# Optimization experiments

Measured on AMD Instinct MI355X. Metric: run time of the kernel, lower is better.

## Reference

```python
import jax, jax.numpy as jnp
import numpy as np

B, S, H, M, E = 64, 512, 1024, 26, 676  # batch, seq, hidden, max_nodes, max_edges (M*M)


def setup_inputs() -> dict:
    key = jax.random.key(0)
    ks = jax.random.split(key, 16)
    seq = jax.random.normal(ks[0], (B, S, H), jnp.float32)
    # ragged, strictly-increasing sentence-end offsets in [1, S-1], zero-padded tail
    rng = np.random.RandomState(0)
    off = np.zeros((B, M - 1), np.int64)
    for b in range(B):
        c = rng.randint(5, M)  # count of valid offsets per sample (ragged)
        off[b, :c] = np.sort(rng.choice(np.arange(1, S), size=c, replace=False))
    s = 1.0 / np.sqrt(H)
    s3 = 1.0 / np.sqrt(3 * H)
    return {
        'sequence_outputs': seq,
        'proof_offsets': jnp.asarray(off),
        'node_labels': jax.random.randint(ks[1], (B, M), 0, 2),
        'edge_labels': jax.random.randint(ks[2], (B, E), 0, 2),
        'W_naf': jax.random.normal(ks[3], (H, H), jnp.float32) * s,
        'b_naf': jnp.zeros((H,), jnp.float32),
        'W_cd': jax.random.normal(ks[4], (H, H), jnp.float32) * s,
        'b_cd': jnp.zeros((H,), jnp.float32),
        'W_co': jax.random.normal(ks[5], (H, 2), jnp.float32) * s,
        'b_co': jnp.zeros((2,), jnp.float32),
        'W_nd': jax.random.normal(ks[6], (H, H), jnp.float32) * s,
        'b_nd': jnp.zeros((H,), jnp.float32),
        'W_no': jax.random.normal(ks[7], (H, 2), jnp.float32) * s,
        'b_no': jnp.zeros((2,), jnp.float32),
        'W_ed': jax.random.normal(ks[8], (3 * H, H), jnp.float32) * s3,
        'b_ed': jnp.zeros((H,), jnp.float32),
        'W_eo': jax.random.normal(ks[9], (H, 2), jnp.float32) * s,
        'b_eo': jnp.zeros((2,), jnp.float32),
    }


def reference(sequence_outputs, proof_offsets, node_labels, edge_labels,
              W_naf, b_naf, W_cd, b_cd, W_co, b_co,
              W_nd, b_nd, W_no, b_no, W_ed, b_ed, W_eo, b_eo):
    Bx, Sx, Hx = sequence_outputs.shape
    Mx = node_labels.shape[1]
    Ex = edge_labels.shape[1]

    cls = sequence_outputs[:, 0, :]                       # [B,H]
    naf = cls @ W_naf + b_naf                             # NAF node embedding
    logits = jnp.tanh(cls @ W_cd + b_cd) @ W_co + b_co    # RobertaClassificationHead (eval: dropout=id)

    # segment-mean pooling via inclusive prefix sums: segment j = tokens (prev_j, off_j]
    P = jnp.cumsum(sequence_outputs, axis=1)              # [B,S,H]
    off = proof_offsets                                   # [B,M-1]
    prev = jnp.concatenate([jnp.zeros((Bx, 1), off.dtype), off[:, :-1]], axis=1)
    valid = off > 0                                       # [B,M-1]
    seg_sum = (jnp.take_along_axis(P, off[..., None], axis=1)
               - jnp.take_along_axis(P, prev[..., None], axis=1))  # [B,M-1,H]
    seg_len = jnp.maximum(off - prev, 1).astype(sequence_outputs.dtype)
    seg_mean = seg_sum / seg_len[..., None] * valid[..., None]

    count = valid.sum(axis=1)                             # nodes per sample (excl. NAF)
    # node embeddings: seg means at 0..count-1, NAF at index count, zeros after
    node_full = jnp.concatenate([seg_mean, jnp.zeros((Bx, 1, Hx), seg_mean.dtype)], axis=1)  # [B,M,H]
    idx = jnp.arange(Mx)
    node_full = node_full + (idx[None, :, None] == count[:, None, None]) * naf[:, None, :]

    # all-pairs edge features over n=count+1 nodes, row-major flat k=i*n+j, zero-padded to E
    n = count + 1                                         # [B]
    k = jnp.arange(Ex)                                    # [E]
    i = jnp.clip(k[None, :] // n[:, None], 0, Mx - 1)     # [B,E]
    j = jnp.clip(k[None, :] % n[:, None], 0, Mx - 1)
    valid_e = (k[None, :] < (n * n)[:, None])[..., None]
    ni = jnp.take_along_axis(node_full, i[..., None], axis=1)  # [B,E,H]
    nj = jnp.take_along_axis(node_full, j[..., None], axis=1)
    edge = jnp.concatenate([nj, ni, nj - ni], axis=-1) * valid_e  # [B,E,3H]

    node_logits = jnp.tanh(node_full @ W_nd + b_nd) @ W_no + b_no
    edge_logits = jnp.tanh(edge @ W_ed + b_ed) @ W_eo + b_eo
    return (logits, node_logits, edge_logits)
```

## Files before the change

### kernel.cpp

```cpp
#include <hip/hip_runtime.h>
#include <hip/hip_bf16.h>

#define B_ 64
#define S_ 512
#define H_ 1024
#define M_ 26
#define E_ 676

typedef short bf16x8 __attribute__((ext_vector_type(8)));
typedef float f32x4 __attribute__((ext_vector_type(4)));

__device__ __forceinline__ void gload16(const void* g, void* l) {
    __builtin_amdgcn_global_load_lds((const __attribute__((address_space(1))) unsigned int*)g,
                                     (__attribute__((address_space(3))) unsigned int*)l,
                                     16, 0, 0);
}

__device__ __forceinline__ float tanh_fast(float x) {
    float e = __expf(2.0f * x);
    return 1.0f - 2.0f * __builtin_amdgcn_rcpf(e + 1.0f);
}

__global__ void k_prep(const float* __restrict__ Wnd, const float* __restrict__ Wed,
                       __hip_bfloat16* __restrict__ Wt) {
    __shared__ float T[32][33];
    int bx = blockIdx.x, by = blockIdx.y, s = blockIdx.z;
    int t = threadIdx.x;
    int c = t & 31, r0 = t >> 5;
    const int HH = H_ * H_;
#pragma unroll
    for (int i = 0; i < 4; ++i) {
        int r = r0 + 8 * i;
        size_t k = by * 32 + r, n = bx * 32 + c;
        float v;
        if (s == 0)      v = Wnd[k * H_ + n];
        else if (s == 1) v = Wed[k * H_ + n] + Wed[2 * HH + k * H_ + n];
        else             v = Wed[HH + k * H_ + n] - Wed[2 * HH + k * H_ + n];
        T[r][c] = v;
    }
    __syncthreads();
#pragma unroll
    for (int i = 0; i < 4; ++i) {
        int rr = r0 + 8 * i;
        Wt[(size_t)(s * H_ + bx * 32 + rr) * H_ + by * 32 + c] = __float2bfloat16(T[c][rr]);
    }
}

__global__ void k_init(const float* __restrict__ bnaf, const float* __restrict__ bcd,
                       float* __restrict__ naf, float* __restrict__ cdh,
                       const int* __restrict__ off, int* __restrict__ count,
                       const float* __restrict__ bed, const float* __restrict__ Weo,
                       const float* __restrict__ beo, float* __restrict__ econ) {
    __shared__ float s0[256], s1[256];
    int bx = blockIdx.x;
    if (bx < 256) {
        int i = bx * 256 + threadIdx.x;
        naf[i] = bnaf[i & (H_ - 1)];
    } else if (bx < 512) {
        int i = (bx - 256) * 256 + threadIdx.x;
        cdh[i] = bcd[i & (H_ - 1)];
    } else if (bx == 512) {
        if (threadIdx.x < 64) {
            int b = threadIdx.x;
            int c = 0;
            for (int m = 0; m < M_ - 1; ++m) c += (off[b * (M_ - 1) + m] > 0) ? 1 : 0;
            count[b] = c;
        }
    } else {
        int tid = threadIdx.x;
        float a0 = 0.f, a1 = 0.f;
        for (int h = tid; h < H_; h += 256) {
            float t = tanh_fast(bed[h]);
            a0 += t * Weo[h * 2 + 0];
            a1 += t * Weo[h * 2 + 1];
        }
        s0[tid] = a0; s1[tid] = a1; __syncthreads();
        for (int o = 128; o > 0; o >>= 1) {
            if (tid < o) { s0[tid] += s0[tid + o]; s1[tid] += s1[tid + o]; }
            __syncthreads();
        }
        if (tid == 0) { econ[0] = s0[0] + beo[0]; econ[1] = s1[0] + beo[1]; }
    }
}

__global__ __launch_bounds__(256) void k_cls2(const float* __restrict__ seq,
                                              const float* __restrict__ Wnaf,
                                              const float* __restrict__ Wcd,
                                              float* __restrict__ naf,
                                              float* __restrict__ cdh) {
    __shared__ float As[16][64];
    __shared__ float Bs[16][64];
    int tid = threadIdx.x;
    int bx = blockIdx.x;
    int kbase = blockIdx.y * 128;
    const float* W;
    float* dst;
    int cbase;
    if (bx < 16) { W = Wnaf; dst = naf; cbase = bx * 64; }
    else         { W = Wcd;  dst = cdh; cbase = (bx - 16) * 64; }
    int tx = tid % 16, ty = tid / 16;
    float c[4][4] = {};
    int la_row = tid / 4;
    int la_k4  = (tid % 4) * 4;
    int lb_k   = tid / 16;
    int lb_c4  = (tid % 16) * 4;
    for (int k0 = 0; k0 < 128; k0 += 16) {
        float4 a = *(const float4*)(seq + (size_t)la_row * S_ * H_ + kbase + k0 + la_k4);
        *(float4*)(&Bs[lb_k][lb_c4]) =
            *(const float4*)(W + (size_t)(kbase + k0 + lb_k) * H_ + cbase + lb_c4);
        As[la_k4 + 0][la_row] = a.x;
        As[la_k4 + 1][la_row] = a.y;
        As[la_k4 + 2][la_row] = a.z;
        As[la_k4 + 3][la_row] = a.w;
        __syncthreads();
#pragma unroll
        for (int kk = 0; kk < 16; ++kk) {
            float4 av = *(const float4*)(&As[kk][ty * 4]);
            float4 bv = *(const float4*)(&Bs[kk][tx * 4]);
            c[0][0] += av.x * bv.x; c[0][1] += av.x * bv.y; c[0][2] += av.x * bv.z; c[0][3] += av.x * bv.w;
            c[1][0] += av.y * bv.x; c[1][1] += av.y * bv.y; c[1][2] += av.y * bv.z; c[1][3] += av.y * bv.w;
            c[2][0] += av.z * bv.x; c[2][1] += av.z * bv.y; c[2][2] += av.z * bv.z; c[2][3] += av.z * bv.w;
            c[3][0] += av.w * bv.x; c[3][1] += av.w * bv.y; c[3][2] += av.w * bv.z; c[3][3] += av.w * bv.w;
        }
        __syncthreads();
    }
#pragma unroll
    for (int i = 0; i < 4; ++i)
#pragma unroll
        for (int j = 0; j < 4; ++j)
            atomicAdd(dst + (size_t)(ty * 4 + i) * H_ + cbase + tx * 4 + j, c[i][j]);
}

__global__ void k_logits(const float* __restrict__ cdh, const float* __restrict__ Wco,
                         const float* __restrict__ bco, float* __restrict__ out) {
    int b = blockIdx.x, tid = threadIdx.x;
    float a0 = 0.f, a1 = 0.f;
    for (int h = tid; h < H_; h += 256) {
        float t = tanh_fast(cdh[(size_t)b * H_ + h]);
        a0 += t * Wco[h * 2 + 0];
        a1 += t * Wco[h * 2 + 1];
    }
    __shared__ float s0[256], s1[256];
    s0[tid] = a0; s1[tid] = a1; __syncthreads();
    for (int o = 128; o > 0; o >>= 1) {
        if (tid < o) { s0[tid] += s0[tid + o]; s1[tid] += s1[tid + o]; }
        __syncthreads();
    }
    if (tid == 0) { out[b * 2 + 0] = s0[0] + bco[0]; out[b * 2 + 1] = s1[0] + bco[1]; }
}

__global__ void k_seg(const float* __restrict__ seq, const int* __restrict__ off,
                      float* __restrict__ node_sum) {
    int b = blockIdx.y;
    int chunk = blockIdx.x;
    __shared__ int offs[M_ - 1];
    __shared__ int c_s, offmax_s;
    int tid = threadIdx.x;
    if (tid < M_ - 1) offs[tid] = off[b * (M_ - 1) + tid];
    __syncthreads();
    if (tid == 0) {
        int c = 0;
        while (c < M_ - 1 && offs[c] > 0) c++;
        c_s = c; offmax_s = (c > 0) ? offs[c - 1] : 0;
    }
    __syncthreads();
    int c = c_s, offmax = offmax_s;
    int t0 = chunk * 32;
    int ts = max(t0, 1), te = min(t0 + 31, offmax);
    if (ts > te) return;
    int m = 0;
    while (m < c && offs[m] < ts) m++;
    const float4* sq = (const float4*)(seq + (size_t)b * S_ * H_);
    float4 acc = make_float4(0, 0, 0, 0);
    for (int t = ts; t <= te; ++t) {
        if (offs[m] < t) {
            float* dst = node_sum + ((size_t)(b * M_ + m)) * H_ + tid * 4;
            atomicAdd(dst + 0, acc.x); atomicAdd(dst + 1, acc.y);
            atomicAdd(dst + 2, acc.z); atomicAdd(dst + 3, acc.w);
            acc = make_float4(0, 0, 0, 0);
            while (offs[m] < t) m++;
        }
        float4 v = sq[(size_t)t * (H_ / 4) + tid];
        acc.x += v.x; acc.y += v.y; acc.z += v.z; acc.w += v.w;
    }
    float* dst = node_sum + ((size_t)(b * M_ + m)) * H_ + tid * 4;
    atomicAdd(dst + 0, acc.x); atomicAdd(dst + 1, acc.y);
    atomicAdd(dst + 2, acc.z); atomicAdd(dst + 3, acc.w);
}

__global__ void k_finalize(const float* __restrict__ sums, const int* __restrict__ off,
                           const int* __restrict__ count, const float* __restrict__ naf,
                           __hip_bfloat16* __restrict__ nodeB) {
    int b = blockIdx.y, m = blockIdx.x, tid = threadIdx.x;
    int cnt = count[b];
    float4 v = make_float4(0, 0, 0, 0);
    const float4* row = (const float4*)(sums + ((size_t)(b * M_ + m)) * H_);
    if (m < M_ - 1) {
        int o = off[b * (M_ - 1) + m];
        if (o > 0) {
            int prev = (m > 0) ? off[b * (M_ - 1) + m - 1] : 0;
            float inv = 1.0f / (float)max(o - prev, 1);
            float4 s = row[tid];
            v = make_float4(s.x * inv, s.y * inv, s.z * inv, s.w * inv);
        }
    }
    if (m == cnt) {
        float4 a = ((const float4*)(naf + (size_t)b * H_))[tid];
        v.x += a.x; v.y += a.y; v.z += a.z; v.w += a.w;
    }
    __hip_bfloat16 __attribute__((aligned(8))) h[4] = {
        __float2bfloat16(v.x), __float2bfloat16(v.y),
        __float2bfloat16(v.z), __float2bfloat16(v.w)};
    *(ushort4*)(nodeB + ((size_t)(b * M_ + m)) * H_ + tid * 4) = *(const ushort4*)h;
}

#define GM 1664
#define GN 3072
#define GK 1024
__global__ __launch_bounds__(256) void k_mfma(const __hip_bfloat16* __restrict__ A,
                                              const __hip_bfloat16* __restrict__ Bt,
                                              float* __restrict__ C) {
    __shared__ __hip_bfloat16 As[128 * 32];
    __shared__ __hip_bfloat16 Bs[128 * 32];
    int tid = threadIdx.x;
    int wid = tid >> 6, ln = tid & 63;
    int row0 = blockIdx.y * 128, col0 = blockIdx.x * 128;
    const __hip_bfloat16* ga = A + (size_t)(row0 + wid * 16 + (ln >> 2)) * GK + (ln & 3) * 8;
    const __hip_bfloat16* gb = Bt + (size_t)(col0 + wid * 16 + (ln >> 2)) * GK + (ln & 3) * 8;
    __hip_bfloat16* lA = As + wid * 512;
    __hip_bfloat16* lB = Bs + wid * 512;
    int mrow = (wid >> 1) * 64, ncol = (wid & 1) * 64;
    int l15 = ln & 15, l4 = ln >> 4;
    f32x4 acc[4][4] = {};
    const __hip_bfloat16* pa = As + (size_t)(mrow + l15) * 32 + l4 * 8;
    const __hip_bfloat16* pb = Bs + (size_t)(ncol + l15) * 32 + l4 * 8;
    for (int k0 = 0; k0 < GK; k0 += 32) {
        gload16(ga, lA);
        gload16(ga + 64 * GK, lA + 2048);
        gload16(gb, lB);
        gload16(gb + 64 * GK, lB + 2048);
        ga += 32; gb += 32;
        __syncthreads();
        bf16x8 af[4], bf[4];
#pragma unroll
        for (int mi = 0; mi < 4; ++mi) af[mi] = *(const bf16x8*)(pa + mi * 16 * 32);
#pragma unroll
        for (int ni = 0; ni < 4; ++ni) bf[ni] = *(const bf16x8*)(pb + ni * 16 * 32);
#pragma unroll
        for (int mi = 0; mi < 4; ++mi)
#pragma unroll
            for (int ni = 0; ni < 4; ++ni)
                acc[mi][ni] = __builtin_amdgcn_mfma_f32_16x16x32_bf16(af[mi], bf[ni],
                                                                      acc[mi][ni], 0, 0, 0);
        __syncthreads();
    }
#pragma unroll
    for (int mi = 0; mi < 4; ++mi)
#pragma unroll
        for (int ni = 0; ni < 4; ++ni) {
            f32x4 v = acc[mi][ni];
            size_t r = row0 + mrow + mi * 16 + l4 * 4;
            size_t cc = col0 + ncol + ni * 16 + l15;
            C[(r + 0) * GN + cc] = v[0];
            C[(r + 1) * GN + cc] = v[1];
            C[(r + 2) * GN + cc] = v[2];
            C[(r + 3) * GN + cc] = v[3];
        }
}

__global__ void k_node_logits(const float* __restrict__ Cm, const float* __restrict__ bnd,
                              const float* __restrict__ Wno, const float* __restrict__ bno,
                              float* __restrict__ out) {
    int r = blockIdx.x * 4 + (threadIdx.x >> 6);
    int lane = threadIdx.x & 63;
    const float4* src = (const float4*)(Cm + (size_t)r * GN);
    float a0 = 0.f, a1 = 0.f;
#pragma unroll
    for (int it = 0; it < 4; ++it) {
        int h = lane * 4 + it * 256;
        float4 s = src[lane + it * 64];
        float4 bb = *(const float4*)(bnd + h);
        float t0 = tanh_fast(s.x + bb.x), t1 = tanh_fast(s.y + bb.y);
        float t2 = tanh_fast(s.z + bb.z), t3 = tanh_fast(s.w + bb.w);
        a0 += t0 * Wno[h * 2 + 0] + t1 * Wno[h * 2 + 2] + t2 * Wno[h * 2 + 4] + t3 * Wno[h * 2 + 6];
        a1 += t0 * Wno[h * 2 + 1] + t1 * Wno[h * 2 + 3] + t2 * Wno[h * 2 + 5] + t3 * Wno[h * 2 + 7];
    }
    for (int o = 32; o > 0; o >>= 1) { a0 += __shfl_down(a0, o); a1 += __shfl_down(a1, o); }
    if (lane == 0) { out[(size_t)r * 2 + 0] = a0 + bno[0]; out[(size_t)r * 2 + 1] = a1 + bno[1]; }
}

__global__ __launch_bounds__(256) void k_edge(const float* __restrict__ Cm,
                                              const int* __restrict__ count,
                                              const float* __restrict__ bed,
                                              const float* __restrict__ Weo,
                                              const float* __restrict__ beo,
                                              const float* __restrict__ econ,
                                              float* __restrict__ out) {
    int b = blockIdx.y;
    int wid = threadIdx.x >> 6, lane = threadIdx.x & 63;
    int wg = blockIdx.x * 4 + wid;
    int n = count[b] + 1;
    int n2 = n * n;
    float4 bed4[4], w04[4], w14[4];
#pragma unroll
    for (int it = 0; it < 4; ++it) {
        int h = lane * 4 + it * 256;
        bed4[it] = *(const float4*)(bed + h);
        w04[it] = make_float4(Weo[h * 2 + 0], Weo[h * 2 + 2], Weo[h * 2 + 4], Weo[h * 2 + 6]);
        w14[it] = make_float4(Weo[h * 2 + 1], Weo[h * 2 + 3], Weo[h * 2 + 5], Weo[h * 2 + 7]);
    }
    float e0 = econ[0], e1 = econ[1];
    float b0 = beo[0], b1 = beo[1];
    for (int k = wg; k < E_; k += 64) {
        float* dst = out + ((size_t)b * E_ + k) * 2;
        if (k >= n2) {
            if (lane == 0) { dst[0] = e0; dst[1] = e1; }
            continue;
        }
        int i = k / n, j = k - i * n;
        const float4* U4 = (const float4*)(Cm + (size_t)(b * M_ + j) * GN + H_);
        const float4* V4 = (const float4*)(Cm + (size_t)(b * M_ + i) * GN + 2 * H_);
        float a0 = 0.f, a1 = 0.f;
#pragma unroll
        for (int it = 0; it < 4; ++it) {
            float4 u = U4[lane + it * 64];
            float4 v = V4[lane + it * 64];
            float t0 = tanh_fast(u.x + v.x + bed4[it].x);
            float t1 = tanh_fast(u.y + v.y + bed4[it].y);
            float t2 = tanh_fast(u.z + v.z + bed4[it].z);
            float t3 = tanh_fast(u.w + v.w + bed4[it].w);
            a0 += t0 * w04[it].x + t1 * w04[it].y + t2 * w04[it].z + t3 * w04[it].w;
            a1 += t0 * w14[it].x + t1 * w14[it].y + t2 * w14[it].z + t3 * w14[it].w;
        }
        for (int o = 32; o > 0; o >>= 1) { a0 += __shfl_down(a0, o); a1 += __shfl_down(a1, o); }
        if (lane == 0) { dst[0] = a0 + b0; dst[1] = a1 + b1; }
    }
}

extern "C" void kernel_launch(void* const* d_in, const int* in_sizes, int n_in,
                              void* d_out, int out_size, void* d_ws, size_t ws_size,
                              hipStream_t stream) {
    const float* seq  = (const float*)d_in[0];
    const int*   off  = (const int*)d_in[1];
    const float* Wnaf = (const float*)d_in[4];  const float* bnaf = (const float*)d_in[5];
    const float* Wcd  = (const float*)d_in[6];  const float* bcd  = (const float*)d_in[7];
    const float* Wco  = (const float*)d_in[8];  const float* bco  = (const float*)d_in[9];
    const float* Wnd  = (const float*)d_in[10]; const float* bnd  = (const float*)d_in[11];
    const float* Wno  = (const float*)d_in[12]; const float* bno  = (const float*)d_in[13];
    const float* Wed  = (const float*)d_in[14]; const float* bed  = (const float*)d_in[15];
    const float* Weo  = (const float*)d_in[16]; const float* beo  = (const float*)d_in[17];
    float* out = (float*)d_out;

    float* ws = (float*)d_ws;
    size_t p = 0;
    float* nodeS = ws + p;  p += (size_t)B_ * M_ * H_;
    float* naf   = ws + p;  p += (size_t)B_ * H_;
    float* cdh   = ws + p;  p += (size_t)B_ * H_;
    __hip_bfloat16* nodeB = (__hip_bfloat16*)(ws + p); p += (size_t)B_ * M_ * H_ / 2;
    __hip_bfloat16* Wt    = (__hip_bfloat16*)(ws + p); p += (size_t)3 * H_ * H_ / 2;
    float* Cbuf  = ws + p;  p += (size_t)B_ * M_ * 3 * H_;
    int*   cnt   = (int*)(ws + p); p += 64;
    float* econ  = ws + p;  p += 2;

    hipMemsetAsync(nodeS, 0, (size_t)B_ * M_ * H_ * sizeof(float), stream);

    k_prep<<<dim3(32, 32, 3), 256, 0, stream>>>(Wnd, Wed, Wt);
    k_init<<<dim3(514), 256, 0, stream>>>(bnaf, bcd, naf, cdh, off, cnt, bed, Weo, beo, econ);
    k_cls2<<<dim3(32, 8), 256, 0, stream>>>(seq, Wnaf, Wcd, naf, cdh);
    k_logits<<<B_, 256, 0, stream>>>(cdh, Wco, bco, out);
    k_seg<<<dim3(16, B_), 256, 0, stream>>>(seq, off, nodeS);
    k_finalize<<<dim3(M_, B_), 256, 0, stream>>>(nodeS, off, cnt, naf, nodeB);
    k_mfma<<<dim3(GN / 128, GM / 128), 256, 0, stream>>>(nodeB, Wt, Cbuf);
    k_node_logits<<<(B_ * M_) / 4, 256, 0, stream>>>(Cbuf, bnd, Wno, bno, out + B_ * 2);
    k_edge<<<dim3(16, B_), 256, 0, stream>>>(Cbuf, cnt, bed, Weo, beo, econ,
                                             out + B_ * 2 + B_ * M_ * 2);
}
```

Baseline: 344.6 us.

## Merge independent kernels into fewer multi-role launches and fold bias init into memset

Combines weight prep, count/econ init, CLS GEMM and segment summation into one launch. Finalize and classification logits become a second launch, and node and edge logits a third, with roles chosen by block index. The per-element bias initialization of naf/cdh is dropped: those buffers are now zeroed by the existing memset and the biases are added where the values are consumed. This cuts the launch count from eight kernels to four. The merged kernels share one shared-memory size and launch bound, and their heterogeneous blocks may schedule unevenly.

```diff
diff --git a/kernel.cpp b/kernel.cpp
--- a/kernel.cpp
+++ b/kernel.cpp
@@ -21,53 +21,50 @@
     return 1.0f - 2.0f * __builtin_amdgcn_rcpf(e + 1.0f);
 }
 
-__global__ void k_prep(const float* __restrict__ Wnd, const float* __restrict__ Wed,
-                       __hip_bfloat16* __restrict__ Wt) {
-    __shared__ float T[32][33];
-    int bx = blockIdx.x, by = blockIdx.y, s = blockIdx.z;
-    int t = threadIdx.x;
-    int c = t & 31, r0 = t >> 5;
-    const int HH = H_ * H_;
-#pragma unroll
-    for (int i = 0; i < 4; ++i) {
-        int r = r0 + 8 * i;
-        size_t k = by * 32 + r, n = bx * 32 + c;
-        float v;
-        if (s == 0)      v = Wnd[k * H_ + n];
-        else if (s == 1) v = Wed[k * H_ + n] + Wed[2 * HH + k * H_ + n];
-        else             v = Wed[HH + k * H_ + n] - Wed[2 * HH + k * H_ + n];
-        T[r][c] = v;
-    }
-    __syncthreads();
-#pragma unroll
-    for (int i = 0; i < 4; ++i) {
-        int rr = r0 + 8 * i;
-        Wt[(size_t)(s * H_ + bx * 32 + rr) * H_ + by * 32 + c] = __float2bfloat16(T[c][rr]);
-    }
-}
-
-__global__ void k_init(const float* __restrict__ bnaf, const float* __restrict__ bcd,
-                       float* __restrict__ naf, float* __restrict__ cdh,
-                       const int* __restrict__ off, int* __restrict__ count,
-                       const float* __restrict__ bed, const float* __restrict__ Weo,
-                       const float* __restrict__ beo, float* __restrict__ econ) {
-    __shared__ float s0[256], s1[256];
-    int bx = blockIdx.x;
-    if (bx < 256) {
-        int i = bx * 256 + threadIdx.x;
-        naf[i] = bnaf[i & (H_ - 1)];
-    } else if (bx < 512) {
-        int i = (bx - 256) * 256 + threadIdx.x;
-        cdh[i] = bcd[i & (H_ - 1)];
-    } else if (bx == 512) {
-        if (threadIdx.x < 64) {
-            int b = threadIdx.x;
+__global__ __launch_bounds__(256) void k_stage1(
+    const float* __restrict__ seq, const int* __restrict__ off,
+    const float* __restrict__ Wnaf, const float* __restrict__ Wcd,
+    const float* __restrict__ Wnd, const float* __restrict__ Wed,
+    const float* __restrict__ bed, const float* __restrict__ Weo,
+    const float* __restrict__ beo,
+    __hip_bfloat16* __restrict__ Wt, int* __restrict__ count,
+    float* __restrict__ econ, float* __restrict__ naf, float* __restrict__ cdh,
+    float* __restrict__ node_sum) {
+    __shared__ float smem[2048];
+    int bid = blockIdx.x;
+    int tid = threadIdx.x;
+
+    if (bid < 3072) {
+        float (*T)[33] = (float(*)[33])smem;
+        int s = bid >> 10, rem = bid & 1023;
+        int bx = rem & 31, by = rem >> 5;
+        int c = tid & 31, r0 = tid >> 5;
+        const int HH = H_ * H_;
+#pragma unroll
+        for (int i = 0; i < 4; ++i) {
+            int r = r0 + 8 * i;
+            size_t k = by * 32 + r, n = bx * 32 + c;
+            float v;
+            if (s == 0)      v = Wnd[k * H_ + n];
+            else if (s == 1) v = Wed[k * H_ + n] + Wed[2 * HH + k * H_ + n];
+            else             v = Wed[HH + k * H_ + n] - Wed[2 * HH + k * H_ + n];
+            T[r][c] = v;
+        }
+        __syncthreads();
+#pragma unroll
+        for (int i = 0; i < 4; ++i) {
+            int rr = r0 + 8 * i;
+            Wt[(size_t)(s * H_ + bx * 32 + rr) * H_ + by * 32 + c] = __float2bfloat16(T[c][rr]);
+        }
+    } else if (bid == 3072) {
+        if (tid < 64) {
+            int b = tid;
             int c = 0;
             for (int m = 0; m < M_ - 1; ++m) c += (off[b * (M_ - 1) + m] > 0) ? 1 : 0;
             count[b] = c;
         }
-    } else {
-        int tid = threadIdx.x;
+    } else if (bid == 3073) {
+        float* s0 = smem; float* s1 = smem + 256;
         float a0 = 0.f, a1 = 0.f;
         for (int h = tid; h < H_; h += 256) {
             float t = tanh_fast(bed[h]);
@@ -80,138 +77,135 @@
             __syncthreads();
         }
         if (tid == 0) { econ[0] = s0[0] + beo[0]; econ[1] = s1[0] + beo[1]; }
+    } else if (bid < 3330) {
+        float (*As)[64] = (float(*)[64])smem;
+        float (*Bs)[64] = (float(*)[64])(smem + 1024);
+        int e = bid - 3074;
+        int bx = e & 31;
+        int kbase = (e >> 5) * 128;
+        const float* W;
+        float* dst;
+        int cbase;
+        if (bx < 16) { W = Wnaf; dst = naf; cbase = bx * 64; }
+        else         { W = Wcd;  dst = cdh; cbase = (bx - 16) * 64; }
+        int tx = tid % 16, ty = tid / 16;
+        float c[4][4] = {};
+        int la_row = tid / 4;
+        int la_k4  = (tid % 4) * 4;
+        int lb_k   = tid / 16;
+        int lb_c4  = (tid % 16) * 4;
+        for (int k0 = 0; k0 < 128; k0 += 16) {
+            float4 a = *(const float4*)(seq + (size_t)la_row * S_ * H_ + kbase + k0 + la_k4);
+            *(float4*)(&Bs[lb_k][lb_c4]) =
+                *(const float4*)(W + (size_t)(kbase + k0 + lb_k) * H_ + cbase + lb_c4);
+            As[la_k4 + 0][la_row] = a.x;
+            As[la_k4 + 1][la_row] = a.y;
+            As[la_k4 + 2][la_row] = a.z;
+            As[la_k4 + 3][la_row] = a.w;
+            __syncthreads();
+#pragma unroll
+            for (int kk = 0; kk < 16; ++kk) {
+                float4 av = *(const float4*)(&As[kk][ty * 4]);
+                float4 bv = *(const float4*)(&Bs[kk][tx * 4]);
+                c[0][0] += av.x * bv.x; c[0][1] += av.x * bv.y; c[0][2] += av.x * bv.z; c[0][3] += av.x * bv.w;
+                c[1][0] += av.y * bv.x; c[1][1] += av.y * bv.y; c[1][2] += av.y * bv.z; c[1][3] += av.y * bv.w;
+                c[2][0] += av.z * bv.x; c[2][1] += av.z * bv.y; c[2][2] += av.z * bv.z; c[2][3] += av.z * bv.w;
+                c[3][0] += av.w * bv.x; c[3][1] += av.w * bv.y; c[3][2] += av.w * bv.z; c[3][3] += av.w * bv.w;
+            }
+            __syncthreads();
+        }
+#pragma unroll
+        for (int i = 0; i < 4; ++i)
+#pragma unroll
+            for (int j = 0; j < 4; ++j)
+                atomicAdd(dst + (size_t)(ty * 4 + i) * H_ + cbase + tx * 4 + j, c[i][j]);
+    } else {
+        int e = bid - 3330;
+        int chunk = e & 15, b = e >> 4;
+        int* offs = (int*)smem;
+        int* cs = (int*)smem + 28;
+        if (tid < M_ - 1) offs[tid] = off[b * (M_ - 1) + tid];
+        __syncthreads();
+        if (tid == 0) {
+            int c = 0;
+            while (c < M_ - 1 && offs[c] > 0) c++;
+            cs[0] = c; cs[1] = (c > 0) ? offs[c - 1] : 0;
+        }
+        __syncthreads();
+        int c = cs[0], offmax = cs[1];
+        int t0 = chunk * 32;
+        int ts = max(t0, 1), te = min(t0 + 31, offmax);
+        if (ts > te) return;
+        int m = 0;
+        while (m < c && offs[m] < ts) m++;
+        const float4* sq = (const float4*)(seq + (size_t)b * S_ * H_);
+        float4 acc = make_float4(0, 0, 0, 0);
+        for (int t = ts; t <= te; ++t) {
+            if (offs[m] < t) {
+                float* dst = node_sum + ((size_t)(b * M_ + m)) * H_ + tid * 4;
+                atomicAdd(dst + 0, acc.x); atomicAdd(dst + 1, acc.y);
+                atomicAdd(dst + 2, acc.z); atomicAdd(dst + 3, acc.w);
+                acc = make_float4(0, 0, 0, 0);
+                while (offs[m] < t) m++;
+            }
+            float4 v = sq[(size_t)t * (H_ / 4) + tid];
+            acc.x += v.x; acc.y += v.y; acc.z += v.z; acc.w += v.w;
+        }
+        float* dst = node_sum + ((size_t)(b * M_ + m)) * H_ + tid * 4;
+        atomicAdd(dst + 0, acc.x); atomicAdd(dst + 1, acc.y);
+        atomicAdd(dst + 2, acc.z); atomicAdd(dst + 3, acc.w);
     }
 }
 
-__global__ __launch_bounds__(256) void k_cls2(const float* __restrict__ seq,
-                                              const float* __restrict__ Wnaf,
-                                              const float* __restrict__ Wcd,
-                                              float* __restrict__ naf,
-                                              float* __restrict__ cdh) {
-    __shared__ float As[16][64];
-    __shared__ float Bs[16][64];
+__global__ __launch_bounds__(256) void k_stage2(
+    const float* __restrict__ sums, const int* __restrict__ off,
+    const int* __restrict__ count, const float* __restrict__ naf,
+    const float* __restrict__ bnaf, __hip_bfloat16* __restrict__ nodeB,
+    const float* __restrict__ cdh, const float* __restrict__ bcd,
+    const float* __restrict__ Wco, const float* __restrict__ bco,
+    float* __restrict__ out) {
+    __shared__ float smem[512];
+    int bid = blockIdx.x;
     int tid = threadIdx.x;
-    int bx = blockIdx.x;
-    int kbase = blockIdx.y * 128;
-    const float* W;
-    float* dst;
-    int cbase;
-    if (bx < 16) { W = Wnaf; dst = naf; cbase = bx * 64; }
-    else         { W = Wcd;  dst = cdh; cbase = (bx - 16) * 64; }
-    int tx = tid % 16, ty = tid / 16;
-    float c[4][4] = {};
-    int la_row = tid / 4;
-    int la_k4  = (tid % 4) * 4;
-    int lb_k   = tid / 16;
-    int lb_c4  = (tid % 16) * 4;
-    for (int k0 = 0; k0 < 128; k0 += 16) {
-        float4 a = *(const float4*)(seq + (size_t)la_row * S_ * H_ + kbase + k0 + la_k4);
-        *(float4*)(&Bs[lb_k][lb_c4]) =
-            *(const float4*)(W + (size_t)(kbase + k0 + lb_k) * H_ + cbase + lb_c4);
-        As[la_k4 + 0][la_row] = a.x;
-        As[la_k4 + 1][la_row] = a.y;
-        As[la_k4 + 2][la_row] = a.z;
-        As[la_k4 + 3][la_row] = a.w;
-        __syncthreads();
-#pragma unroll
-        for (int kk = 0; kk < 16; ++kk) {
-            float4 av = *(const float4*)(&As[kk][ty * 4]);
-            float4 bv = *(const float4*)(&Bs[kk][tx * 4]);
-            c[0][0] += av.x * bv.x; c[0][1] += av.x * bv.y; c[0][2] += av.x * bv.z; c[0][3] += av.x * bv.w;
-            c[1][0] += av.y * bv.x; c[1][1] += av.y * bv.y; c[1][2] += av.y * bv.z; c[1][3] += av.y * bv.w;
-            c[2][0] += av.z * bv.x; c[2][1] += av.z * bv.y; c[2][2] += av.z * bv.z; c[2][3] += av.z * bv.w;
-            c[3][0] += av.w * bv.x; c[3][1] += av.w * bv.y; c[3][2] += av.w * bv.z; c[3][3] += av.w * bv.w;
-        }
-        __syncthreads();
+    if (bid < 1664) {
+        int b = bid / 26, m = bid - b * 26;
+        int cnt = count[b];
+        float4 v = make_float4(0, 0, 0, 0);
+        const float4* row = (const float4*)(sums + ((size_t)(b * M_ + m)) * H_);
+        if (m < M_ - 1) {
+            int o = off[b * (M_ - 1) + m];
+            if (o > 0) {
+                int prev = (m > 0) ? off[b * (M_ - 1) + m - 1] : 0;
+                float inv = 1.0f / (float)max(o - prev, 1);
+                float4 s = row[tid];
+                v = make_float4(s.x * inv, s.y * inv, s.z * inv, s.w * inv);
+            }
+        }
+        if (m == cnt) {
+            float4 a = ((const float4*)(naf + (size_t)b * H_))[tid];
+            float4 bb = ((const float4*)bnaf)[tid];
+            v.x += a.x + bb.x; v.y += a.y + bb.y; v.z += a.z + bb.z; v.w += a.w + bb.w;
+        }
+        __hip_bfloat16 __attribute__((aligned(8))) h[4] = {
+            __float2bfloat16(v.x), __float2bfloat16(v.y),
+            __float2bfloat16(v.z), __float2bfloat16(v.w)};
+        *(ushort4*)(nodeB + ((size_t)(b * M_ + m)) * H_ + tid * 4) = *(const ushort4*)h;
+    } else {
+        int b = bid - 1664;
+        float* s0 = smem; float* s1 = smem + 256;
+        float a0 = 0.f, a1 = 0.f;
+        for (int h = tid; h < H_; h += 256) {
+            float t = tanh_fast(cdh[(size_t)b * H_ + h] + bcd[h]);
+            a0 += t * Wco[h * 2 + 0];
+            a1 += t * Wco[h * 2 + 1];
+        }
+        s0[tid] = a0; s1[tid] = a1; __syncthreads();
+        for (int o = 128; o > 0; o >>= 1) {
+            if (tid < o) { s0[tid] += s0[tid + o]; s1[tid] += s1[tid + o]; }
+            __syncthreads();
+        }
+        if (tid == 0) { out[b * 2 + 0] = s0[0] + bco[0]; out[b * 2 + 1] = s1[0] + bco[1]; }
     }
-#pragma unroll
-    for (int i = 0; i < 4; ++i)
-#pragma unroll
-        for (int j = 0; j < 4; ++j)
-            atomicAdd(dst + (size_t)(ty * 4 + i) * H_ + cbase + tx * 4 + j, c[i][j]);
-}
-
-__global__ void k_logits(const float* __restrict__ cdh, const float* __restrict__ Wco,
-                         const float* __restrict__ bco, float* __restrict__ out) {
-    int b = blockIdx.x, tid = threadIdx.x;
-    float a0 = 0.f, a1 = 0.f;
-    for (int h = tid; h < H_; h += 256) {
-        float t = tanh_fast(cdh[(size_t)b * H_ + h]);
-        a0 += t * Wco[h * 2 + 0];
-        a1 += t * Wco[h * 2 + 1];
-    }
-    __shared__ float s0[256], s1[256];
-    s0[tid] = a0; s1[tid] = a1; __syncthreads();
-    for (int o = 128; o > 0; o >>= 1) {
-        if (tid < o) { s0[tid] += s0[tid + o]; s1[tid] += s1[tid + o]; }
-        __syncthreads();
-    }
-    if (tid == 0) { out[b * 2 + 0] = s0[0] + bco[0]; out[b * 2 + 1] = s1[0] + bco[1]; }
-}
-
-__global__ void k_seg(const float* __restrict__ seq, const int* __restrict__ off,
-                      float* __restrict__ node_sum) {
-    int b = blockIdx.y;
-    int chunk = blockIdx.x;
-    __shared__ int offs[M_ - 1];
-    __shared__ int c_s, offmax_s;
-    int tid = threadIdx.x;
-    if (tid < M_ - 1) offs[tid] = off[b * (M_ - 1) + tid];
-    __syncthreads();
-    if (tid == 0) {
-        int c = 0;
-        while (c < M_ - 1 && offs[c] > 0) c++;
-        c_s = c; offmax_s = (c > 0) ? offs[c - 1] : 0;
-    }
-    __syncthreads();
-    int c = c_s, offmax = offmax_s;
-    int t0 = chunk * 32;
-    int ts = max(t0, 1), te = min(t0 + 31, offmax);
-    if (ts > te) return;
-    int m = 0;
-    while (m < c && offs[m] < ts) m++;
-    const float4* sq = (const float4*)(seq + (size_t)b * S_ * H_);
-    float4 acc = make_float4(0, 0, 0, 0);
-    for (int t = ts; t <= te; ++t) {
-        if (offs[m] < t) {
-            float* dst = node_sum + ((size_t)(b * M_ + m)) * H_ + tid * 4;
-            atomicAdd(dst + 0, acc.x); atomicAdd(dst + 1, acc.y);
-            atomicAdd(dst + 2, acc.z); atomicAdd(dst + 3, acc.w);
-            acc = make_float4(0, 0, 0, 0);
-            while (offs[m] < t) m++;
-        }
-        float4 v = sq[(size_t)t * (H_ / 4) + tid];
-        acc.x += v.x; acc.y += v.y; acc.z += v.z; acc.w += v.w;
-    }
-    float* dst = node_sum + ((size_t)(b * M_ + m)) * H_ + tid * 4;
-    atomicAdd(dst + 0, acc.x); atomicAdd(dst + 1, acc.y);
-    atomicAdd(dst + 2, acc.z); atomicAdd(dst + 3, acc.w);
-}
-
-__global__ void k_finalize(const float* __restrict__ sums, const int* __restrict__ off,
-                           const int* __restrict__ count, const float* __restrict__ naf,
-                           __hip_bfloat16* __restrict__ nodeB) {
-    int b = blockIdx.y, m = blockIdx.x, tid = threadIdx.x;
-    int cnt = count[b];
-    float4 v = make_float4(0, 0, 0, 0);
-    const float4* row = (const float4*)(sums + ((size_t)(b * M_ + m)) * H_);
-    if (m < M_ - 1) {
-        int o = off[b * (M_ - 1) + m];
-        if (o > 0) {
-            int prev = (m > 0) ? off[b * (M_ - 1) + m - 1] : 0;
-            float inv = 1.0f / (float)max(o - prev, 1);
-            float4 s = row[tid];
-            v = make_float4(s.x * inv, s.y * inv, s.z * inv, s.w * inv);
-        }
-    }
-    if (m == cnt) {
-        float4 a = ((const float4*)(naf + (size_t)b * H_))[tid];
-        v.x += a.x; v.y += a.y; v.z += a.z; v.w += a.w;
-    }
-    __hip_bfloat16 __attribute__((aligned(8))) h[4] = {
-        __float2bfloat16(v.x), __float2bfloat16(v.y),
-        __float2bfloat16(v.z), __float2bfloat16(v.w)};
-    *(ushort4*)(nodeB + ((size_t)(b * M_ + m)) * H_ + tid * 4) = *(const ushort4*)h;
 }
 
 #define GM 1664
@@ -268,72 +262,71 @@
         }
 }
 
-__global__ void k_node_logits(const float* __restrict__ Cm, const float* __restrict__ bnd,
-                              const float* __restrict__ Wno, const float* __restrict__ bno,
-                              float* __restrict__ out) {
-    int r = blockIdx.x * 4 + (threadIdx.x >> 6);
-    int lane = threadIdx.x & 63;
-    const float4* src = (const float4*)(Cm + (size_t)r * GN);
-    float a0 = 0.f, a1 = 0.f;
-#pragma unroll
-    for (int it = 0; it < 4; ++it) {
-        int h = lane * 4 + it * 256;
-        float4 s = src[lane + it * 64];
-        float4 bb = *(const float4*)(bnd + h);
-        float t0 = tanh_fast(s.x + bb.x), t1 = tanh_fast(s.y + bb.y);
-        float t2 = tanh_fast(s.z + bb.z), t3 = tanh_fast(s.w + bb.w);
-        a0 += t0 * Wno[h * 2 + 0] + t1 * Wno[h * 2 + 2] + t2 * Wno[h * 2 + 4] + t3 * Wno[h * 2 + 6];
-        a1 += t0 * Wno[h * 2 + 1] + t1 * Wno[h * 2 + 3] + t2 * Wno[h * 2 + 5] + t3 * Wno[h * 2 + 7];
-    }
-    for (int o = 32; o > 0; o >>= 1) { a0 += __shfl_down(a0, o); a1 += __shfl_down(a1, o); }
-    if (lane == 0) { out[(size_t)r * 2 + 0] = a0 + bno[0]; out[(size_t)r * 2 + 1] = a1 + bno[1]; }
-}
-
-__global__ __launch_bounds__(256) void k_edge(const float* __restrict__ Cm,
-                                              const int* __restrict__ count,
-                                              const float* __restrict__ bed,
-                                              const float* __restrict__ Weo,
-                                              const float* __restrict__ beo,
-                                              const float* __restrict__ econ,
-                                              float* __restrict__ out) {
-    int b = blockIdx.y;
+__global__ __launch_bounds__(256) void k_stage4(
+    const float* __restrict__ Cm, const int* __restrict__ count,
+    const float* __restrict__ bnd, const float* __restrict__ Wno,
+    const float* __restrict__ bno, const float* __restrict__ bed,
+    const float* __restrict__ Weo, const float* __restrict__ beo,
+    const float* __restrict__ econ, float* __restrict__ out_n,
+    float* __restrict__ out_e) {
+    int bid = blockIdx.x;
     int wid = threadIdx.x >> 6, lane = threadIdx.x & 63;
-    int wg = blockIdx.x * 4 + wid;
-    int n = count[b] + 1;
-    int n2 = n * n;
-    float4 bed4[4], w04[4], w14[4];
-#pragma unroll
-    for (int it = 0; it < 4; ++it) {
-        int h = lane * 4 + it * 256;
-        bed4[it] = *(const float4*)(bed + h);
-        w04[it] = make_float4(Weo[h * 2 + 0], Weo[h * 2 + 2], Weo[h * 2 + 4], Weo[h * 2 + 6]);
-        w14[it] = make_float4(Weo[h * 2 + 1], Weo[h * 2 + 3], Weo[h * 2 + 5], Weo[h * 2 + 7]);
-    }
-    float e0 = econ[0], e1 = econ[1];
-    float b0 = beo[0], b1 = beo[1];
-    for (int k = wg; k < E_; k += 64) {
-        float* dst = out + ((size_t)b * E_ + k) * 2;
-        if (k >= n2) {
-            if (lane == 0) { dst[0] = e0; dst[1] = e1; }
-            continue;
-        }
-        int i = k / n, j = k - i * n;
-        const float4* U4 = (const float4*)(Cm + (size_t)(b * M_ + j) * GN + H_);
-        const float4* V4 = (const float4*)(Cm + (size_t)(b * M_ + i) * GN + 2 * H_);
+    if (bid < 416) {
+        int r = bid * 4 + wid;
+        const float4* src = (const float4*)(Cm + (size_t)r * GN);
         float a0 = 0.f, a1 = 0.f;
 #pragma unroll
         for (int it = 0; it < 4; ++it) {
-            float4 u = U4[lane + it * 64];
-            float4 v = V4[lane + it * 64];
-            float t0 = tanh_fast(u.x + v.x + bed4[it].x);
-            float t1 = tanh_fast(u.y + v.y + bed4[it].y);
-            float t2 = tanh_fast(u.z + v.z + bed4[it].z);
-            float t3 = tanh_fast(u.w + v.w + bed4[it].w);
-            a0 += t0 * w04[it].x + t1 * w04[it].y + t2 * w04[it].z + t3 * w04[it].w;
-            a1 += t0 * w14[it].x + t1 * w14[it].y + t2 * w14[it].z + t3 * w14[it].w;
+            int h = lane * 4 + it * 256;
+            float4 s = src[lane + it * 64];
+            float4 bb = *(const float4*)(bnd + h);
+            float t0 = tanh_fast(s.x + bb.x), t1 = tanh_fast(s.y + bb.y);
+            float t2 = tanh_fast(s.z + bb.z), t3 = tanh_fast(s.w + bb.w);
+            a0 += t0 * Wno[h * 2 + 0] + t1 * Wno[h * 2 + 2] + t2 * Wno[h * 2 + 4] + t3 * Wno[h * 2 + 6];
+            a1 += t0 * Wno[h * 2 + 1] + t1 * Wno[h * 2 + 3] + t2 * Wno[h * 2 + 5] + t3 * Wno[h * 2 + 7];
         }
         for (int o = 32; o > 0; o >>= 1) { a0 += __shfl_down(a0, o); a1 += __shfl_down(a1, o); }
-        if (lane == 0) { dst[0] = a0 + b0; dst[1] = a1 + b1; }
+        if (lane == 0) { out_n[(size_t)r * 2 + 0] = a0 + bno[0]; out_n[(size_t)r * 2 + 1] = a1 + bno[1]; }
+    } else {
+        int e = bid - 416;
+        int b = e >> 4;
+        int wg = (e & 15) * 4 + wid;
+        int n = count[b] + 1;
+        int n2 = n * n;
+        float4 bed4[4], w04[4], w14[4];
+#pragma unroll
+        for (int it = 0; it < 4; ++it) {
+            int h = lane * 4 + it * 256;
+            bed4[it] = *(const float4*)(bed + h);
+            w04[it] = make_float4(Weo[h * 2 + 0], Weo[h * 2 + 2], Weo[h * 2 + 4], Weo[h * 2 + 6]);
+            w14[it] = make_float4(Weo[h * 2 + 1], Weo[h * 2 + 3], Weo[h * 2 + 5], Weo[h * 2 + 7]);
+        }
+        float e0 = econ[0], e1 = econ[1];
+        float b0 = beo[0], b1 = beo[1];
+        for (int k = wg; k < E_; k += 64) {
+            float* dst = out_e + ((size_t)b * E_ + k) * 2;
+            if (k >= n2) {
+                if (lane == 0) { dst[0] = e0; dst[1] = e1; }
+                continue;
+            }
+            int i = k / n, j = k - i * n;
+            const float4* U4 = (const float4*)(Cm + (size_t)(b * M_ + j) * GN + H_);
+            const float4* V4 = (const float4*)(Cm + (size_t)(b * M_ + i) * GN + 2 * H_);
+            float a0 = 0.f, a1 = 0.f;
+#pragma unroll
+            for (int it = 0; it < 4; ++it) {
+                float4 u = U4[lane + it * 64];
+                float4 v = V4[lane + it * 64];
+                float t0 = tanh_fast(u.x + v.x + bed4[it].x);
+                float t1 = tanh_fast(u.y + v.y + bed4[it].y);
+                float t2 = tanh_fast(u.z + v.z + bed4[it].z);
+                float t3 = tanh_fast(u.w + v.w + bed4[it].w);
+                a0 += t0 * w04[it].x + t1 * w04[it].y + t2 * w04[it].z + t3 * w04[it].w;
+                a1 += t0 * w14[it].x + t1 * w14[it].y + t2 * w14[it].z + t3 * w14[it].w;
+            }
+            for (int o = 32; o > 0; o >>= 1) { a0 += __shfl_down(a0, o); a1 += __shfl_down(a1, o); }
+            if (lane == 0) { dst[0] = a0 + b0; dst[1] = a1 + b1; }
+        }
     }
 }
 
@@ -362,16 +355,14 @@
     int*   cnt   = (int*)(ws + p); p += 64;
     float* econ  = ws + p;  p += 2;
 
-    hipMemsetAsync(nodeS, 0, (size_t)B_ * M_ * H_ * sizeof(float), stream);
-
-    k_prep<<<dim3(32, 32, 3), 256, 0, stream>>>(Wnd, Wed, Wt);
-    k_init<<<dim3(514), 256, 0, stream>>>(bnaf, bcd, naf, cdh, off, cnt, bed, Weo, beo, econ);
-    k_cls2<<<dim3(32, 8), 256, 0, stream>>>(seq, Wnaf, Wcd, naf, cdh);
-    k_logits<<<B_, 256, 0, stream>>>(cdh, Wco, bco, out);
-    k_seg<<<dim3(16, B_), 256, 0, stream>>>(seq, off, nodeS);
-    k_finalize<<<dim3(M_, B_), 256, 0, stream>>>(nodeS, off, cnt, naf, nodeB);
+    hipMemsetAsync(nodeS, 0, ((size_t)B_ * M_ * H_ + 2 * (size_t)B_ * H_) * sizeof(float),
+                   stream);
+
+    k_stage1<<<dim3(4354), 256, 0, stream>>>(seq, off, Wnaf, Wcd, Wnd, Wed, bed, Weo, beo,
+                                             Wt, cnt, econ, naf, cdh, nodeS);
+    k_stage2<<<dim3(1728), 256, 0, stream>>>(nodeS, off, cnt, naf, bnaf, nodeB,
+                                             cdh, bcd, Wco, bco, out);
     k_mfma<<<dim3(GN / 128, GM / 128), 256, 0, stream>>>(nodeB, Wt, Cbuf);
-    k_node_logits<<<(B_ * M_) / 4, 256, 0, stream>>>(Cbuf, bnd, Wno, bno, out + B_ * 2);
-    k_edge<<<dim3(16, B_), 256, 0, stream>>>(Cbuf, cnt, bed, Weo, beo, econ,
-                                             out + B_ * 2 + B_ * M_ * 2);
-}
+    k_stage4<<<dim3(1440), 256, 0, stream>>>(Cbuf, cnt, bnd, Wno, bno, bed, Weo, beo, econ,
+                                             out + B_ * 2, out + B_ * 2 + B_ * M_ * 2);
+}
```

After: 311.1 us. -9.7%, faster.
